# Kernel tuning notes

Hardware: AMD Instinct MI355X
Metric: run time of the kernel (lower is better)

Reference implementation:

```python
import jax, jax.numpy as jnp
import numpy as np

VOCAB, E, H, OUT = 24, 16, 32, 2
B, T = 16384, 128


def setup_inputs() -> dict:
    key = jax.random.key(0)
    ks = jax.random.split(key, 8)
    x = jax.random.randint(ks[0], (B, T), 0, VOCAB, dtype=jnp.int32)
    emb = jax.random.normal(ks[1], (VOCAB, E), dtype=jnp.float32) * 0.1
    emb = emb.at[0].set(0.0)  # padding_idx=0
    s = 1.0 / np.sqrt(H)
    W_ih = jax.random.uniform(ks[2], (4 * H, E), minval=-s, maxval=s, dtype=jnp.float32)
    W_hh = jax.random.uniform(ks[3], (4 * H, H), minval=-s, maxval=s, dtype=jnp.float32)
    b_ih = jax.random.uniform(ks[4], (4 * H,), minval=-s, maxval=s, dtype=jnp.float32)
    b_hh = jax.random.uniform(ks[5], (4 * H,), minval=-s, maxval=s, dtype=jnp.float32)
    sf = 1.0 / np.sqrt(H)
    fc_w = jax.random.uniform(ks[6], (OUT, H), minval=-sf, maxval=sf, dtype=jnp.float32)
    fc_b = jax.random.uniform(ks[7], (OUT,), minval=-sf, maxval=sf, dtype=jnp.float32)
    return {"x": x, "emb": emb, "W_ih": W_ih, "W_hh": W_hh,
            "b_ih": b_ih, "b_hh": b_hh, "fc_w": fc_w, "fc_b": fc_b}


def _lstm_last_h(xe, W_ih, W_hh, b_ih, b_hh):
    # xe: [B, T, E]. PyTorch gate order: i, f, g, o.
    b = xe.shape[0]
    # Precompute input projections for all timesteps in one GEMM: [B, T, 4H]
    gates_x = jnp.einsum('bte,ge->btg', xe, W_ih) + (b_ih + b_hh)

    def step(carry, gx_t):
        h, c = carry
        gates = gx_t + h @ W_hh.T  # [B, 4H]
        i, f, g, o = jnp.split(gates, 4, axis=-1)
        i = jax.nn.sigmoid(i)
        f = jax.nn.sigmoid(f)
        g = jnp.tanh(g)
        o = jax.nn.sigmoid(o)
        c = f * c + i * g
        h = o * jnp.tanh(c)
        return (h, c), None

    h0 = jnp.zeros((b, W_hh.shape[1]), dtype=xe.dtype)
    c0 = jnp.zeros_like(h0)
    (h_last, _), _ = jax.lax.scan(step, (h0, c0), jnp.swapaxes(gates_x, 0, 1))
    return h_last  # == lstm_outputs[:, -1, :]


def reference(x, emb, W_ih, W_hh, b_ih, b_hh, fc_w, fc_b):
    xe = emb[x]                                   # [B, T, E] embedding lookup
    h_last = _lstm_last_h(xe, W_ih, W_hh, b_ih, b_hh)  # [B, H]
    return h_last @ fc_w.T + fc_b                 # [B, 2]
```

## Files before the change

kernel.cpp:

```cpp
#include <hip/hip_runtime.h>
#include <hip/hip_bf16.h>

typedef __bf16 bf16x8 __attribute__((ext_vector_type(8)));
typedef float  f32x4  __attribute__((ext_vector_type(4)));

#define VOCAB 24
#define EDIM  16
#define HDIM  32
#define TLEN  128

union A2U { int4 w; bf16x8 v; };

__device__ __forceinline__ float ex2(float x)  { return __builtin_amdgcn_exp2f(x); }
__device__ __forceinline__ float rcpf_(float x){ return __builtin_amdgcn_rcpf(x); }

__global__ __launch_bounds__(64) void lstm_fused(
    const int*   __restrict__ x,
    const float* __restrict__ emb,
    const float* __restrict__ W_ih,
    const float* __restrict__ W_hh,
    const float* __restrict__ b_ih,
    const float* __restrict__ b_hh,
    const float* __restrict__ fc_w,
    const float* __restrict__ fc_b,
    float*       __restrict__ out)
{
    __shared__ __align__(16) float fbuf[16][33];

    const int lane  = threadIdx.x;
    const int l15   = lane & 15;
    const int hi    = lane >> 4;
    const int kbase = hi * 8;
    const int kh    = hi * 4;
    const int row0  = blockIdx.x * 16;

    bf16x8 b1f[8];
    bf16x8 b2f[8];
    #pragma unroll
    for (int nt = 0; nt < 8; ++nt) {
        const int g    = nt >> 1;
        const int jcol = 8 * (l15 >> 2) + (l15 & 3) + 4 * (nt & 1);
        const int gcol = g * 32 + jcol;
        const float scale = (g == 2) ? -2.88539008f : -1.44269504f;
        const float* wrow = W_hh + gcol * HDIM;
        #pragma unroll
        for (int i = 0; i < 8; ++i)
            b1f[nt][i] = (__bf16)(scale * wrow[kbase + i]);
        const float bias = b_ih[gcol] + b_hh[gcol];
        const float* wi = W_ih + gcol * EDIM;
        #pragma unroll
        for (int i = 0; i < 8; ++i) {
            const int v = kbase + i;
            float s = 0.0f;
            if (v < VOCAB) {
                s = bias;
                #pragma unroll
                for (int e = 0; e < EDIM; ++e)
                    s += emb[v * EDIM + e] * wi[e];
            }
            b2f[nt][i] = (__bf16)(scale * s);
        }
    }

    float d[8];
    #pragma unroll
    for (int q = 0; q < 8; ++q) d[q] = 0.0f;

    f32x4 p[8];
    bf16x8 hb;
    #pragma unroll
    for (int i = 0; i < 8; ++i) hb[i] = (__bf16)0.0f;

    const f32x4 z = {0.f, 0.f, 0.f, 0.f};
    const int* xrow = x + (row0 + l15) * TLEN;

#define PRECOMP(XV) do {                                                       \
    const int xv_   = (XV);                                                    \
    const int hotw_ = 0x3F80 << ((xv_ & 1) << 4);                              \
    const int hoth_ = xv_ >> 1;                                                \
    A2U a2_;                                                                   \
    a2_.w.x = (hoth_ == kh + 0) ? hotw_ : 0;                                   \
    a2_.w.y = (hoth_ == kh + 1) ? hotw_ : 0;                                   \
    a2_.w.z = (hoth_ == kh + 2) ? hotw_ : 0;                                   \
    a2_.w.w = (hoth_ == kh + 3) ? hotw_ : 0;                                   \
    _Pragma("unroll")                                                          \
    for (int nt = 0; nt < 8; ++nt)                                             \
        p[nt] = __builtin_amdgcn_mfma_f32_16x16x32_bf16(b2f[nt], a2_.v, z, 0, 0, 0); \
} while (0)

#define SLOT(FIRST, LAST, XVN) do {                                            \
    f32x4 acc_[8];                                                             \
    if (FIRST) {                                                               \
        _Pragma("unroll")                                                      \
        for (int nt = 0; nt < 8; ++nt) acc_[nt] = p[nt];                       \
    } else {                                                                   \
        _Pragma("unroll")                                                      \
        for (int nt = 0; nt < 8; ++nt)                                         \
            acc_[nt] = __builtin_amdgcn_mfma_f32_16x16x32_bf16(b1f[nt], hb, p[nt], 0, 0, 0); \
    }                                                                          \
                                \
    float ea_[8], ew_[8], eb_[8], ev_[8];                                      \
    _Pragma("unroll")                                                          \
    for (int k = 0; k < 8; ++k) {                                              \
        const int qq_ = k >> 2, r_ = k & 3;                                    \
        ea_[k] = ex2(acc_[qq_    ][r_]);                                \
        ew_[k] = ex2(acc_[qq_ + 2][r_]);                                \
        eb_[k] = ex2(acc_[qq_ + 4][r_]);                     \
        ev_[k] = ex2(acc_[qq_ + 6][r_]);                                \
    }                                                                          \
                          \
    float TP_[8], N_[8], dd_[8];                                               \
    _Pragma("unroll")                                                          \
    for (int k = 0; k < 8; ++k) {                                              \
        const float P_ = (1.0f + ea_[k]) * (1.0f + eb_[k]);                    \
        const float T_ = 1.0f + ew_[k];                                        \
        const float G_ = fmaf(2.88539008f, eb_[k], -2.88539008f);              \
        TP_[k] = T_ * P_;                                                      \
        N_[k]  = fmaf(d[k], P_, G_ * T_);                                      \
    }                                                                          \
    _Pragma("unroll")                                                          \
    for (int kp = 0; kp < 4; ++kp) {                                           \
        const int k0 = 2 * kp, k1 = 2 * kp + 1;                                \
        const float xr = rcpf_(TP_[k0] * TP_[k1]);                             \
        dd_[k0] = fminf(N_[k0] * xr * TP_[k1], 40.0f);                         \
        dd_[k1] = fminf(N_[k1] * xr * TP_[k0], 40.0f);                         \
        d[k0] = dd_[k0];                                                       \
        d[k1] = dd_[k1];                                                       \
    }                                                                          \
                                 \
    float eu_[8], U_[8];                                                       \
    _Pragma("unroll")                                                          \
    for (int k = 0; k < 8; ++k) {                                              \
        eu_[k] = ex2(dd_[k]);                                                  \
        U_[k]  = (1.0f + ev_[k]) * (1.0f + eu_[k]);                            \
    }                                                                          \
    _Pragma("unroll")                                                          \
    for (int kp = 0; kp < 4; ++kp) {                                           \
        const int k0 = 2 * kp, k1 = 2 * kp + 1;                                \
        const float yr = rcpf_(U_[k0] * U_[k1]);                               \
        const float hv0 = (1.0f - eu_[k0]) * yr * U_[k1];                      \
        const float hv1 = (1.0f - eu_[k1]) * yr * U_[k0];                      \
        if (!(LAST)) {                                                         \
            hb[k0] = (__bf16)hv0;                                              \
            hb[k1] = (__bf16)hv1;                                              \
        } else {                                                               \
            fbuf[l15][kbase + k0] = hv0;                                       \
            fbuf[l15][kbase + k1] = hv1;                                       \
        }                                                                      \
    }                                                                          \
    if (!(LAST)) PRECOMP(XVN);                          \
} while (0)

    int4 q0 = *(const int4*)xrow;
    int4 xq = *(const int4*)(xrow + 4);
    PRECOMP(q0.x);

    SLOT(true,  false, q0.y);
    SLOT(false, false, q0.z);
    SLOT(false, false, q0.w);
    SLOT(false, false, xq.x);

    #pragma unroll 1
    for (int t = 4; t < 124; t += 4) {
        const int4 n = *(const int4*)(xrow + t + 4);
        SLOT(false, false, xq.y);
        SLOT(false, false, xq.z);
        SLOT(false, false, xq.w);
        SLOT(false, false, n.x);
        xq = n;
    }

    SLOT(false, false, xq.y);
    SLOT(false, false, xq.z);
    SLOT(false, false, xq.w);
    SLOT(false, true,  0);

#undef SLOT
#undef PRECOMP

    __syncthreads();

    if (lane < 16) {
        float o0 = fc_b[0], o1 = fc_b[1];
        #pragma unroll
        for (int jj = 0; jj < HDIM; ++jj) {
            const float h = fbuf[lane][jj];
            o0 += fc_w[jj]        * h;
            o1 += fc_w[HDIM + jj] * h;
        }
        float2 res;
        res.x = o0; res.y = o1;
        *(float2*)&out[(row0 + lane) * 2] = res;
    }
}

extern "C" void kernel_launch(void* const* d_in, const int* in_sizes, int n_in,
                              void* d_out, int out_size, void* d_ws, size_t ws_size,
                              hipStream_t stream) {
    const int*   x    = (const int*)  d_in[0];
    const float* emb  = (const float*)d_in[1];
    const float* W_ih = (const float*)d_in[2];
    const float* W_hh = (const float*)d_in[3];
    const float* b_ih = (const float*)d_in[4];
    const float* b_hh = (const float*)d_in[5];
    const float* fc_w = (const float*)d_in[6];
    const float* fc_b = (const float*)d_in[7];
    float* out = (float*)d_out;

    const int B    = in_sizes[0] / TLEN;
    const int nblk = B / 16;

    lstm_fused<<<nblk, 64, 0, stream>>>(x, emb, W_ih, W_hh, b_ih, b_hh, fc_w, fc_b, out);
}
```

Baseline: 102.3 us.

## Split recurrent MFMA into two K16 halves to overlap gate math with matmul

Replaces the single 16x16x32 recurrent MFMA per gate tile with two 16x16x16 MFMAs over the low and high halves of the hidden state. Gate columns are remapped so each half of the gate outputs produces exactly the hidden elements needed by the next step's corresponding K-half. The low-half matmul for the next step can then be issued while the second half's nonlinearities are still being computed, shortening the serial dependency chain per timestep. It doubles the MFMA instruction count and adds an extra live accumulator set, which raises register pressure.

```diff
diff --git a/kernel.cpp b/kernel.cpp
--- a/kernel.cpp
+++ b/kernel.cpp
@@ -2,6 +2,8 @@
 #include <hip/hip_bf16.h>
 
 typedef __bf16 bf16x8 __attribute__((ext_vector_type(8)));
+typedef __bf16 bf16x4 __attribute__((ext_vector_type(4)));
+typedef short  s16x4  __attribute__((ext_vector_type(4)));
 typedef float  f32x4  __attribute__((ext_vector_type(4)));
 
 #define VOCAB 24
@@ -10,9 +12,15 @@
 #define TLEN  128
 
 union A2U { int4 w; bf16x8 v; };
+union H4U { bf16x4 h; s16x4 s; };
 
 __device__ __forceinline__ float ex2(float x)  { return __builtin_amdgcn_exp2f(x); }
 __device__ __forceinline__ float rcpf_(float x){ return __builtin_amdgcn_rcpf(x); }
+
+__device__ __forceinline__ f32x4 mfma_k16(bf16x4 a, bf16x4 b, f32x4 c) {
+    H4U ua, ub; ua.h = a; ub.h = b;
+    return __builtin_amdgcn_mfma_f32_16x16x16bf16_1k(ua.s, ub.s, c, 0, 0, 0);
+}
 
 __global__ __launch_bounds__(64) void lstm_fused(
     const int*   __restrict__ x,
@@ -31,21 +39,23 @@
     const int l15   = lane & 15;
     const int hi    = lane >> 4;
     const int kbase = hi * 8;
+    const int k4    = hi * 4;
     const int kh    = hi * 4;
     const int row0  = blockIdx.x * 16;
 
-    bf16x8 b1f[8];
+    bf16x4 b1lo[8], b1hi[8];
     bf16x8 b2f[8];
     #pragma unroll
     for (int nt = 0; nt < 8; ++nt) {
         const int g    = nt >> 1;
-        const int jcol = 8 * (l15 >> 2) + (l15 & 3) + 4 * (nt & 1);
-        const int gcol = g * 32 + jcol;
+        const int gcol = g * 32 + l15 + 16 * (nt & 1);
         const float scale = (g == 2) ? -2.88539008f : -1.44269504f;
         const float* wrow = W_hh + gcol * HDIM;
         #pragma unroll
-        for (int i = 0; i < 8; ++i)
-            b1f[nt][i] = (__bf16)(scale * wrow[kbase + i]);
+        for (int i = 0; i < 4; ++i) {
+            b1lo[nt][i] = (__bf16)(scale * wrow[k4 + i]);
+            b1hi[nt][i] = (__bf16)(scale * wrow[16 + k4 + i]);
+        }
         const float bias = b_ih[gcol] + b_hh[gcol];
         const float* wi = W_ih + gcol * EDIM;
         #pragma unroll
@@ -67,9 +77,10 @@
     for (int q = 0; q < 8; ++q) d[q] = 0.0f;
 
     f32x4 p[8];
-    bf16x8 hb;
-    #pragma unroll
-    for (int i = 0; i < 8; ++i) hb[i] = (__bf16)0.0f;
+    f32x4 accLo[8];
+    bf16x4 hbl, hbh;
+    #pragma unroll
+    for (int i = 0; i < 4; ++i) { hbl[i] = (__bf16)0.0f; hbh[i] = (__bf16)0.0f; }
 
     const f32x4 z = {0.f, 0.f, 0.f, 0.f};
     const int* xrow = x + (row0 + l15) * TLEN;
@@ -88,94 +99,98 @@
         p[nt] = __builtin_amdgcn_mfma_f32_16x16x32_bf16(b2f[nt], a2_.v, z, 0, 0, 0); \
 } while (0)
 
-#define SLOT(FIRST, LAST, XVN) do {                                            \
-    f32x4 acc_[8];                                                             \
-    if (FIRST) {                                                               \
-        _Pragma("unroll")                                                      \
-        for (int nt = 0; nt < 8; ++nt) acc_[nt] = p[nt];                       \
-    } else {                                                                   \
-        _Pragma("unroll")                                                      \
-        for (int nt = 0; nt < 8; ++nt)                                         \
-            acc_[nt] = __builtin_amdgcn_mfma_f32_16x16x32_bf16(b1f[nt], hb, p[nt], 0, 0, 0); \
-    }                                                                          \
-                                \
-    float ea_[8], ew_[8], eb_[8], ev_[8];                                      \
-    _Pragma("unroll")                                                          \
-    for (int k = 0; k < 8; ++k) {                                              \
-        const int qq_ = k >> 2, r_ = k & 3;                                    \
-        ea_[k] = ex2(acc_[qq_    ][r_]);                                \
-        ew_[k] = ex2(acc_[qq_ + 2][r_]);                                \
-        eb_[k] = ex2(acc_[qq_ + 4][r_]);                     \
-        ev_[k] = ex2(acc_[qq_ + 6][r_]);                                \
-    }                                                                          \
-                          \
-    float TP_[8], N_[8], dd_[8];                                               \
-    _Pragma("unroll")                                                          \
-    for (int k = 0; k < 8; ++k) {                                              \
-        const float P_ = (1.0f + ea_[k]) * (1.0f + eb_[k]);                    \
-        const float T_ = 1.0f + ew_[k];                                        \
-        const float G_ = fmaf(2.88539008f, eb_[k], -2.88539008f);              \
-        TP_[k] = T_ * P_;                                                      \
-        N_[k]  = fmaf(d[k], P_, G_ * T_);                                      \
-    }                                                                          \
-    _Pragma("unroll")                                                          \
-    for (int kp = 0; kp < 4; ++kp) {                                           \
-        const int k0 = 2 * kp, k1 = 2 * kp + 1;                                \
+#define GHALF(H, LAST) do {                                                    \
+    float ea_[4], ew_[4], eb_[4], ev_[4];                                      \
+    _Pragma("unroll")                                                          \
+    for (int s = 0; s < 4; ++s) {                                              \
+        ea_[s] = ex2(acc_[(H)    ][s]);                                 \
+        ew_[s] = ex2(acc_[(H) + 2][s]);                                 \
+        eb_[s] = ex2(acc_[(H) + 4][s]);                      \
+        ev_[s] = ex2(acc_[(H) + 6][s]);                                 \
+    }                                                                          \
+    float TP_[4], N_[4], dd_[4];                                               \
+    _Pragma("unroll")                                                          \
+    for (int s = 0; s < 4; ++s) {                                              \
+        const float P_ = (1.0f + ea_[s]) * (1.0f + eb_[s]);                    \
+        const float T_ = 1.0f + ew_[s];                                        \
+        const float G_ = fmaf(2.88539008f, eb_[s], -2.88539008f);              \
+        TP_[s] = T_ * P_;                                                      \
+        N_[s]  = fmaf(d[4 * (H) + s], P_, G_ * T_);                            \
+    }                                                                          \
+    _Pragma("unroll")                                                          \
+    for (int sp = 0; sp < 2; ++sp) {                                           \
+        const int k0 = 2 * sp, k1 = 2 * sp + 1;                                \
         const float xr = rcpf_(TP_[k0] * TP_[k1]);                             \
         dd_[k0] = fminf(N_[k0] * xr * TP_[k1], 40.0f);                         \
         dd_[k1] = fminf(N_[k1] * xr * TP_[k0], 40.0f);                         \
-        d[k0] = dd_[k0];                                                       \
-        d[k1] = dd_[k1];                                                       \
-    }                                                                          \
-                                 \
-    float eu_[8], U_[8];                                                       \
-    _Pragma("unroll")                                                          \
-    for (int k = 0; k < 8; ++k) {                                              \
-        eu_[k] = ex2(dd_[k]);                                                  \
-        U_[k]  = (1.0f + ev_[k]) * (1.0f + eu_[k]);                            \
-    }                                                                          \
-    _Pragma("unroll")                                                          \
-    for (int kp = 0; kp < 4; ++kp) {                                           \
-        const int k0 = 2 * kp, k1 = 2 * kp + 1;                                \
-        const float yr = rcpf_(U_[k0] * U_[k1]);                               \
+        d[4 * (H) + k0] = dd_[k0];                                             \
+        d[4 * (H) + k1] = dd_[k1];                                             \
+    }                                                                          \
+    float eu_[4], U_[4];                                                       \
+    _Pragma("unroll")                                                          \
+    for (int s = 0; s < 4; ++s) {                                              \
+        eu_[s] = ex2(dd_[s]);                                                  \
+        U_[s]  = (1.0f + ev_[s]) * (1.0f + eu_[s]);                            \
+    }                                                                          \
+    _Pragma("unroll")                                                          \
+    for (int sp = 0; sp < 2; ++sp) {                                           \
+        const int k0 = 2 * sp, k1 = 2 * sp + 1;                                \
+        const float yr  = rcpf_(U_[k0] * U_[k1]);                              \
         const float hv0 = (1.0f - eu_[k0]) * yr * U_[k1];                      \
         const float hv1 = (1.0f - eu_[k1]) * yr * U_[k0];                      \
         if (!(LAST)) {                                                         \
-            hb[k0] = (__bf16)hv0;                                              \
-            hb[k1] = (__bf16)hv1;                                              \
+            if (H) { hbh[k0] = (__bf16)hv0; hbh[k1] = (__bf16)hv1; }           \
+            else   { hbl[k0] = (__bf16)hv0; hbl[k1] = (__bf16)hv1; }           \
         } else {                                                               \
-            fbuf[l15][kbase + k0] = hv0;                                       \
-            fbuf[l15][kbase + k1] = hv1;                                       \
+            fbuf[l15][4 * hi + k0 + 16 * (H)] = hv0;                           \
+            fbuf[l15][4 * hi + k1 + 16 * (H)] = hv1;                           \
         }                                                                      \
     }                                                                          \
-    if (!(LAST)) PRECOMP(XVN);                          \
+} while (0)
+
+#define SLOT(LAST, XVN) do {                                                   \
+    f32x4 acc_[8];                                                             \
+    _Pragma("unroll")                                                          \
+    for (int nt = 0; nt < 8; ++nt)                                             \
+        acc_[nt] = mfma_k16(b1hi[nt], hbh, accLo[nt]);       \
+    GHALF(0, LAST);                                      \
+    if (!(LAST)) {                                                             \
+        PRECOMP(XVN);                                        \
+        _Pragma("unroll")                                                      \
+        for (int nt = 0; nt < 8; ++nt)                                         \
+            accLo[nt] = mfma_k16(b1lo[nt], hbl, p[nt]);    \
+    }                                                                          \
+    GHALF(1, LAST);                                      \
 } while (0)
 
     int4 q0 = *(const int4*)xrow;
     int4 xq = *(const int4*)(xrow + 4);
     PRECOMP(q0.x);
-
-    SLOT(true,  false, q0.y);
-    SLOT(false, false, q0.z);
-    SLOT(false, false, q0.w);
-    SLOT(false, false, xq.x);
+    #pragma unroll
+    for (int nt = 0; nt < 8; ++nt) accLo[nt] = p[nt];
+
+    SLOT(false, q0.y);
+    SLOT(false, q0.z);
+    SLOT(false, q0.w);
+    SLOT(false, xq.x);
 
     #pragma unroll 1
     for (int t = 4; t < 124; t += 4) {
         const int4 n = *(const int4*)(xrow + t + 4);
-        SLOT(false, false, xq.y);
-        SLOT(false, false, xq.z);
-        SLOT(false, false, xq.w);
-        SLOT(false, false, n.x);
+        SLOT(false, xq.y);
+        SLOT(false, xq.z);
+        SLOT(false, xq.w);
+        SLOT(false, n.x);
         xq = n;
     }
 
-    SLOT(false, false, xq.y);
-    SLOT(false, false, xq.z);
-    SLOT(false, false, xq.w);
-    SLOT(false, true,  0);
+    SLOT(false, xq.y);
+    SLOT(false, xq.z);
+    SLOT(false, xq.w);
+    SLOT(true,  0);
 
 #undef SLOT
+#undef GHALF
 #undef PRECOMP
 
     __syncthreads();
```

Result: no change. 102.3 us (-0.0%).
